# Performance work log

Measured on AMD Instinct MI355X. Metric: run time of the kernel, lower is better.

The kernel has to match this reference:

```python
import jax, jax.numpy as jnp
import numpy as np

B, C, H, W = 16, 256, 64, 64
NUM_HEADS = 4
GROUPS = 8
EPS = 1e-5


def setup_inputs() -> dict:
    key = jax.random.key(0)
    ks = jax.random.split(key, 7)
    x = jax.random.normal(ks[0], (B, C, H, W), dtype=jnp.float32)
    # GroupNorm affine params (torch default: weight=1, bias=0; randomize slightly for a stronger test)
    norm_w = jnp.ones((C,), jnp.float32) + 0.1 * jax.random.normal(ks[1], (C,), jnp.float32)
    norm_b = 0.1 * jax.random.normal(ks[2], (C,), jnp.float32)
    # 1x1 convs == channel GEMMs; kaiming-uniform-ish init scale
    s = 1.0 / np.sqrt(C)
    qkv_w = jax.random.uniform(ks[3], (3 * C, C), jnp.float32, -s, s)
    qkv_b = jax.random.uniform(ks[4], (3 * C,), jnp.float32, -s, s)
    proj_w = jax.random.uniform(ks[5], (C, C), jnp.float32, -s, s)
    proj_b = jax.random.uniform(ks[6], (C,), jnp.float32, -s, s)
    return {"x": x, "norm_w": norm_w, "norm_b": norm_b,
            "qkv_w": qkv_w, "qkv_b": qkv_b, "proj_w": proj_w, "proj_b": proj_b}


def reference(x, norm_w, norm_b, qkv_w, qkv_b, proj_w, proj_b):
    b, c, h, w = x.shape
    nh = NUM_HEADS
    dh = c // nh
    n = h * w
    # GroupNorm(8, C)
    xg = x.reshape(b, GROUPS, c // GROUPS, h, w)
    mean = xg.mean(axis=(2, 3, 4), keepdims=True)
    var = xg.var(axis=(2, 3, 4), keepdims=True)
    xn = ((xg - mean) * jax.lax.rsqrt(var + EPS)).reshape(b, c, h, w)
    xn = xn * norm_w[None, :, None, None] + norm_b[None, :, None, None]
    # QKV 1x1 conv as channel GEMM
    qkv = jnp.einsum('bchw,oc->bohw', xn, qkv_w) + qkv_b[None, :, None, None]
    qkv = qkv.reshape(b, 3, nh, dh, n)
    q, k, v = qkv[:, 0], qkv[:, 1], qkv[:, 2]  # each (B, nh, dh, N)
    scale = dh ** (-0.5)
    # Faithful to original einsum labeling: contracts over spatial axis,
    # attention matrix is over the HEADS axis: attn (B, dh, nh, nh)
    attn = jnp.einsum('bnhd,bmhd->bhnm', q * scale, k)
    attn = jax.nn.softmax(attn, axis=-1)
    out = jnp.einsum('bhnm,bmhd->bnhd', attn, v).reshape(b, c, h, w)
    return jnp.einsum('bchw,oc->bohw', out, proj_w) + proj_b[None, :, None, None] + x
```

## Files before the change

kernel.cpp:

```cpp
#include <hip/hip_runtime.h>
#include <stdint.h>

#define BB 16
#define CC 256
#define PP 4096

typedef __attribute__((ext_vector_type(4))) float f32x4;
typedef __attribute__((ext_vector_type(8))) short bf16x8;

static __device__ __forceinline__ float bf2f(unsigned short u) {
    union { uint32_t i; float f; } w; w.i = ((uint32_t)u) << 16; return w.f;
}
static __device__ __forceinline__ unsigned short f2bf(float f) {
    union { float f; uint32_t i; } w; w.f = f;
    uint32_t u = w.i;
    uint32_t r = u + 0x7FFFu + ((u >> 16) & 1u);
    return (unsigned short)(r >> 16);
}
static __device__ __forceinline__ float dot4(f32x4 a, f32x4 b) {
    return a.x * b.x + a.y * b.y + a.z * b.z + a.w * b.w;
}

static __device__ __forceinline__ void gl2lds16(const void* g, void* l) {
    __builtin_amdgcn_global_load_lds(
        (const __attribute__((address_space(1))) void*)g,
        (__attribute__((address_space(3))) void*)l, 16, 0, 0);
}

__global__ void gn_partial_k(const float* __restrict__ x, float* __restrict__ Sx,
                             float* __restrict__ Sxx) {
    int ch0 = blockIdx.x * 8;
    int t = threadIdx.x;
    int lc = t >> 5, l32 = t & 31;
    int ch = ch0 + lc;
    const f32x4* v = (const f32x4*)(x + (size_t)ch * PP);
    float s = 0.f, ss = 0.f;
    for (int i = l32; i < PP / 4; i += 32) {
        f32x4 tv = v[i];
        s  += tv.x + tv.y + tv.z + tv.w;
        ss += tv.x * tv.x + tv.y * tv.y + tv.z * tv.z + tv.w * tv.w;
    }
    for (int off = 16; off > 0; off >>= 1) {
        s  += __shfl_down(s, off, 32);
        ss += __shfl_down(ss, off, 32);
    }
    if (l32 == 0) { Sx[ch] = s; Sxx[ch] = ss; }
}

__global__ void gn_final_k(const float* __restrict__ Sx, const float* __restrict__ Sxx,
                           const float* __restrict__ nw, const float* __restrict__ nb,
                           float* __restrict__ a_s, float* __restrict__ b_s,
                           float* __restrict__ s_vec) {
    int b = blockIdx.x, c = threadIdx.x;
    __shared__ float lsx[256], lsxx[256];
    float mySx = Sx[b * CC + c];
    lsx[c] = mySx; lsxx[c] = Sxx[b * CC + c];
    __syncthreads();
    int g0 = (c >> 5) << 5;
    float S = 0.f, SS = 0.f;
    for (int j = 0; j < 32; j++) { S += lsx[g0 + j]; SS += lsxx[g0 + j]; }
    const float inv = 1.0f / 131072.0f;
    float mean = S * inv;
    float var = SS * inv - mean * mean;
    float rstd = rsqrtf(var + 1e-5f);
    float w = nw[c];
    float a = rstd * w;
    float sh = nb[c] - mean * rstd * w;
    a_s[b * CC + c] = a;
    b_s[b * CC + c] = sh;
    s_vec[b * CC + c] = a * mySx + 4096.0f * sh;
}

__global__ void cvt_bf16_k(const float* __restrict__ in, unsigned short* __restrict__ out, int n) {
    int i = blockIdx.x * 256 + threadIdx.x;
    if (i < n) out[i] = f2bf(in[i]);
}

__global__ void xnt_k(const float* __restrict__ x, const float* __restrict__ a_s,
                      const float* __restrict__ b_s, unsigned short* __restrict__ xnT,
                      unsigned short* __restrict__ xnC) {
    int pt = blockIdx.x & 63, ct = (blockIdx.x >> 6) & 3, b = blockIdx.x >> 8;
    int c0 = ct * 64, p0 = pt * 64;
    __shared__ unsigned short T[64][66];
    int t = threadIdx.x;
    int cl = t >> 4, pl4 = (t & 15) * 4;
    for (int i = 0; i < 4; i++) {
        int c = c0 + i * 16 + cl;
        float a = a_s[b * CC + c], sh = b_s[b * CC + c];
        f32x4 v = *(const f32x4*)(x + ((size_t)b * CC + c) * PP + p0 + pl4);
        ushort4 u;
        u.x = f2bf(a * v.x + sh);
        u.y = f2bf(a * v.y + sh);
        u.z = f2bf(a * v.z + sh);
        u.w = f2bf(a * v.w + sh);
        T[i * 16 + cl][pl4 + 0] = u.x;
        T[i * 16 + cl][pl4 + 1] = u.y;
        T[i * 16 + cl][pl4 + 2] = u.z;
        T[i * 16 + cl][pl4 + 3] = u.w;
        *(ushort4*)(xnC + ((size_t)b * CC + c) * PP + p0 + pl4) = u;
    }
    __syncthreads();
    int pl = t >> 2, c16 = (t & 3) * 16;
    union { unsigned short h[16]; uint4 u[2]; } buf;
    for (int j = 0; j < 16; j++) buf.h[j] = T[c16 + j][pl];
    unsigned short* dst = xnT + ((size_t)b * PP + p0 + pl) * CC + c0 + c16;
    *(uint4*)dst       = buf.u[0];
    *(uint4*)(dst + 8) = buf.u[1];
}

static __device__ __forceinline__ void gemm_core(const unsigned short* __restrict__ Rg,
                                                 const unsigned short* __restrict__ Cg,
                                                 int kLen, int rstride,
                                                 f32x4 (&acc)[4][4]) {
    __shared__ unsigned short Rs[128][32];
    __shared__ unsigned short Cs[128][32];
    int t = threadIdx.x;
    int lane = t & 63, wave = t >> 6;
    int wm = wave >> 1, wn = wave & 1;
    int lr = lane & 15, lq = lane >> 4;
    int srow = t >> 2;
    int ssl = (((t & 3) ^ ((t >> 3) & 3))) * 8;
    int fsw = (lr >> 1) & 3;
    for (int mi = 0; mi < 4; mi++)
        for (int ni = 0; ni < 4; ni++) {
            acc[mi][ni][0] = 0.f; acc[mi][ni][1] = 0.f;
            acc[mi][ni][2] = 0.f; acc[mi][ni][3] = 0.f;
        }
    const unsigned short* gr0 = Rg + (size_t)srow * rstride + ssl;
    const unsigned short* gr1 = gr0 + (size_t)64 * rstride;
    const unsigned short* gc0 = Cg + (size_t)srow * rstride + ssl;
    const unsigned short* gc1 = gc0 + (size_t)64 * rstride;
    char* dr0 = (char*)&Rs[0][0] + t * 16;
    char* dr1 = dr0 + 4096;
    char* dc0 = (char*)&Cs[0][0] + t * 16;
    char* dc1 = dc0 + 4096;
    for (int k0 = 0; k0 < kLen; k0 += 32) {
        __syncthreads();
        gl2lds16(gr0 + k0, dr0);
        gl2lds16(gr1 + k0, dr1);
        gl2lds16(gc0 + k0, dc0);
        gl2lds16(gc1 + k0, dc1);
        __syncthreads();
        bf16x8 af[4], bfr[4];
        for (int mi = 0; mi < 4; mi++)
            af[mi]  = *(const bf16x8*)&Rs[wm * 64 + mi * 16 + lr][(lq ^ fsw) * 8];
        for (int ni = 0; ni < 4; ni++)
            bfr[ni] = *(const bf16x8*)&Cs[wn * 64 + ni * 16 + lr][(lq ^ fsw) * 8];
        for (int mi = 0; mi < 4; mi++)
            for (int ni = 0; ni < 4; ni++)
                acc[mi][ni] = __builtin_amdgcn_mfma_f32_16x16x32_bf16(af[mi], bfr[ni], acc[mi][ni], 0, 0, 0);
    }
}

__global__ __launch_bounds__(256) void v_gemm_k(const unsigned short* __restrict__ Wvb,
                                                const unsigned short* __restrict__ xnT,
                                                const float* __restrict__ qkv_b,
                                                unsigned short* __restrict__ vT) {
    int nt = blockIdx.x & 31;
    int rest = blockIdx.x >> 5;
    int mt = rest & 1;
    int b  = rest >> 1;
    int c0 = mt * 128, p0 = nt * 128;
    f32x4 acc[4][4];
    gemm_core(Wvb + (size_t)c0 * 256, xnT + ((size_t)b * PP + p0) * 256, 256, 256, acc);
    int t = threadIdx.x, lane = t & 63, wave = t >> 6;
    int wm = wave >> 1, wn = wave & 1, lr = lane & 15, lq = lane >> 4;
    for (int mi = 0; mi < 4; mi++) {
        int c4 = c0 + wm * 64 + mi * 16 + lq * 4;
        f32x4 bias = *(const f32x4*)(qkv_b + 512 + c4);
        for (int ni = 0; ni < 4; ni++) {
            int p = p0 + wn * 64 + ni * 16 + lr;
            ushort4 u;
            u.x = f2bf(acc[mi][ni][0] + bias.x);
            u.y = f2bf(acc[mi][ni][1] + bias.y);
            u.z = f2bf(acc[mi][ni][2] + bias.z);
            u.w = f2bf(acc[mi][ni][3] + bias.w);
            *(ushort4*)(vT + ((size_t)b * PP + p) * CC + c4) = u;
        }
    }
}

__global__ __launch_bounds__(256) void gram_k(const unsigned short* __restrict__ xnC,
                                              float* __restrict__ Gpart) {
    int pc  = blockIdx.x & 7;
    int t12 = (blockIdx.x >> 3) & 3;
    int b   = blockIdx.x >> 5;
    int t1 = (t12 >> 1) * 128;
    int t2 = (t12 & 1) * 128;
    f32x4 acc[4][4];
    gemm_core(xnC + ((size_t)b * CC + t2) * PP + pc * 512,
              xnC + ((size_t)b * CC + t1) * PP + pc * 512, 512, PP, acc);
    int t = threadIdx.x, lane = t & 63, wave = t >> 6;
    int wm = wave >> 1, wn = wave & 1, lr = lane & 15, lq = lane >> 4;
    float* dst = Gpart + ((size_t)(pc * 16 + b)) * 65536;
    for (int mi = 0; mi < 4; mi++) {
        int c2q = t2 + wm * 64 + mi * 16 + lq * 4;
        for (int ni = 0; ni < 4; ni++) {
            int c1 = t1 + wn * 64 + ni * 16 + lr;
            *(f32x4*)(dst + (size_t)c1 * 256 + c2q) = acc[mi][ni];
        }
    }
}

__global__ void greduce_k(const float* __restrict__ Gpart, unsigned short* __restrict__ Gb) {
    int i = blockIdx.x * 256 + threadIdx.x;
    float s = 0.f;
    for (int pc = 0; pc < 8; pc++) s += Gpart[(size_t)pc * 16 * 65536 + i];
    Gb[i] = f2bf(s);
}

__global__ __launch_bounds__(256) void u_gemm_k(const unsigned short* __restrict__ Gb,
                                                const unsigned short* __restrict__ Wqkvb,
                                                float* __restrict__ UT) {
    int t12 = blockIdx.x & 3, b = blockIdx.x >> 2;
    int t1 = (t12 >> 1) * 128;
    int t2 = (t12 & 1) * 128;
    f32x4 acc[4][4];
    gemm_core(Gb + ((size_t)b * 256 + t1) * 256,
              Wqkvb + (size_t)(256 + t2) * 256, 256, 256, acc);
    int t = threadIdx.x, lane = t & 63, wave = t >> 6;
    int wm = wave >> 1, wn = wave & 1, lr = lane & 15, lq = lane >> 4;
    for (int mi = 0; mi < 4; mi++) {
        int c1q = t1 + wm * 64 + mi * 16 + lq * 4;
        for (int ni = 0; ni < 4; ni++) {
            int kr = t2 + wn * 64 + ni * 16 + lr;
            *(f32x4*)(UT + ((size_t)b * 256 + kr) * 256 + c1q) = acc[mi][ni];
        }
    }
}

__global__ void scoresfin_k(const float* __restrict__ qkv_w, const float* __restrict__ qkv_b,
                            const float* __restrict__ UT, const float* __restrict__ s_vec,
                            float* __restrict__ attn) {
    int h = blockIdx.x & 63, b = blockIdx.x >> 6;
    int l = threadIdx.x;
    int c = l * 4;
    f32x4 sv = *(const f32x4*)(s_vec + b * CC + c);
    f32x4 wq[4], wk[4], ut[4];
    for (int n = 0; n < 4; n++) wq[n] = *(const f32x4*)(qkv_w + (size_t)(n * 64 + h) * 256 + c);
    for (int m = 0; m < 4; m++) wk[m] = *(const f32x4*)(qkv_w + (size_t)(256 + m * 64 + h) * 256 + c);
    for (int m = 0; m < 4; m++) ut[m] = *(const f32x4*)(UT + ((size_t)b * 256 + m * 64 + h) * 256 + c);
    float red[24];
    for (int n = 0; n < 4; n++)
        for (int m = 0; m < 4; m++) red[n * 4 + m] = dot4(wq[n], ut[m]);
    for (int n = 0; n < 4; n++) red[16 + n] = dot4(wq[n], sv);
    for (int m = 0; m < 4; m++) red[20 + m] = dot4(wk[m], sv);
    #pragma unroll
    for (int i = 0; i < 24; i++)
        for (int off = 32; off > 0; off >>= 1)
            red[i] += __shfl_xor(red[i], off);
    __shared__ float sred[24];
    if (l == 0)
        for (int i = 0; i < 24; i++) sred[i] = red[i];
    __syncthreads();
    if (l < 4) {
        int n = l;
        float bq = qkv_b[n * 64 + h];
        float dqn = sred[16 + n];
        float lg[4];
        for (int m = 0; m < 4; m++) {
            float bk = qkv_b[256 + m * 64 + h];
            lg[m] = 0.125f * (sred[n * 4 + m] + bq * sred[20 + m] + bk * dqn + 4096.0f * bq * bk);
        }
        float mx = fmaxf(fmaxf(lg[0], lg[1]), fmaxf(lg[2], lg[3]));
        float e0 = expf(lg[0] - mx), e1 = expf(lg[1] - mx);
        float e2 = expf(lg[2] - mx), e3 = expf(lg[3] - mx);
        float inv = 1.0f / (e0 + e1 + e2 + e3);
        float* dst = attn + ((size_t)(b * 64 + h) * 4 + n) * 4;
        dst[0] = e0 * inv; dst[1] = e1 * inv; dst[2] = e2 * inv; dst[3] = e3 * inv;
    }
}

__global__ void make_wp_k(const float* __restrict__ proj_w, const float* __restrict__ attn,
                          unsigned short* __restrict__ Wp) {
    int t = threadIdx.x;
    int o = blockIdx.x & 255, b = blockIdx.x >> 8;
    int m = t >> 6, hh = t & 63;
    float s = 0.f;
    for (int n = 0; n < 4; n++)
        s += proj_w[o * 256 + n * 64 + hh] * attn[((size_t)(b * 64 + hh) * 4 + n) * 4 + m];
    Wp[((size_t)b * 256 + o) * 256 + t] = f2bf(s);
}

__global__ __launch_bounds__(256) void final_gemm_k(const unsigned short* __restrict__ Wp,
                                                    const unsigned short* __restrict__ vT,
                                                    const float* __restrict__ proj_b,
                                                    const float* __restrict__ x,
                                                    float* __restrict__ out) {
    int nt = blockIdx.x & 31;
    int rest = blockIdx.x >> 5;
    int mt = rest & 1;
    int b  = rest >> 1;
    int o0 = mt * 128, p0 = nt * 128;
    f32x4 acc[4][4];
    gemm_core(vT + ((size_t)b * PP + p0) * 256, Wp + ((size_t)b * 256 + o0) * 256, 256, 256, acc);
    int t = threadIdx.x, lane = t & 63, wave = t >> 6;
    int wm = wave >> 1, wn = wave & 1, lr = lane & 15, lq = lane >> 4;
    for (int mi = 0; mi < 4; mi++) {
        int p4 = p0 + wm * 64 + mi * 16 + lq * 4;
        for (int ni = 0; ni < 4; ni++) {
            int o = o0 + wn * 64 + ni * 16 + lr;
            size_t idx = ((size_t)b * CC + o) * PP + p4;
            float bias = proj_b[o];
            f32x4 xv = *(const f32x4*)(x + idx);
            f32x4 r;
            r[0] = acc[mi][ni][0] + bias + xv[0];
            r[1] = acc[mi][ni][1] + bias + xv[1];
            r[2] = acc[mi][ni][2] + bias + xv[2];
            r[3] = acc[mi][ni][3] + bias + xv[3];
            *(f32x4*)(out + idx) = r;
        }
    }
}

extern "C" void kernel_launch(void* const* d_in, const int* in_sizes, int n_in,
                              void* d_out, int out_size, void* d_ws, size_t ws_size,
                              hipStream_t stream) {
    const float* x      = (const float*)d_in[0];
    const float* norm_w = (const float*)d_in[1];
    const float* norm_b = (const float*)d_in[2];
    const float* qkv_w  = (const float*)d_in[3];
    const float* qkv_b  = (const float*)d_in[4];
    const float* proj_w = (const float*)d_in[5];
    const float* proj_b = (const float*)d_in[6];
    float* out = (float*)d_out;

    char* ws = (char*)d_ws;
    size_t off = 0;
    auto alloc = [&](size_t bytes) {
        void* p = ws + off;
        off += (bytes + 255) & ~(size_t)255;
        return p;
    };
    float* Sx    = (float*)alloc(BB * CC * sizeof(float));
    float* Sxx   = (float*)alloc(BB * CC * sizeof(float));
    float* a_s   = (float*)alloc(BB * CC * sizeof(float));
    float* b_s   = (float*)alloc(BB * CC * sizeof(float));
    float* s_vec = (float*)alloc(BB * CC * sizeof(float));
    float* attn  = (float*)alloc((size_t)BB * 64 * 16 * sizeof(float));
    unsigned short* Wqkvb = (unsigned short*)alloc((size_t)768 * 256 * 2);
    unsigned short* Wp    = (unsigned short*)alloc((size_t)BB * 256 * 256 * 2);
    unsigned short* Gb    = (unsigned short*)alloc((size_t)BB * 65536 * 2);
    float*          UT    = (float*)alloc((size_t)BB * 65536 * 4);
    float*          Gpart = (float*)alloc((size_t)8 * BB * 65536 * 4);
    unsigned short* xnT   = (unsigned short*)alloc((size_t)BB * PP * CC * 2);
    unsigned short* xnC   = (unsigned short*)alloc((size_t)BB * PP * CC * 2);
    unsigned short* vT    = (unsigned short*)alloc((size_t)BB * PP * CC * 2);

    gn_partial_k<<<BB * CC / 8, 256, 0, stream>>>(x, Sx, Sxx);
    gn_final_k<<<BB, 256, 0, stream>>>(Sx, Sxx, norm_w, norm_b, a_s, b_s, s_vec);
    cvt_bf16_k<<<768, 256, 0, stream>>>(qkv_w, Wqkvb, 768 * 256);
    xnt_k<<<4096, 256, 0, stream>>>(x, a_s, b_s, xnT, xnC);
    v_gemm_k<<<BB * 2 * 32, 256, 0, stream>>>(Wqkvb + 512 * 256, xnT, qkv_b, vT);
    gram_k<<<BB * 4 * 8, 256, 0, stream>>>(xnC, Gpart);
    greduce_k<<<BB * 65536 / 256, 256, 0, stream>>>(Gpart, Gb);
    u_gemm_k<<<BB * 4, 256, 0, stream>>>(Gb, Wqkvb, UT);
    scoresfin_k<<<BB * 64, 64, 0, stream>>>(qkv_w, qkv_b, UT, s_vec, attn);
    make_wp_k<<<BB * 256, 256, 0, stream>>>(proj_w, attn, Wp);
    final_gemm_k<<<BB * 2 * 32, 256, 0, stream>>>(Wp, vT, proj_b, x, out);
}
```

Measured before the change: 270.2 us.

## Fold V projection into per-batch output weights and drop the V GEMM

Removes the separate V GEMM and its bf16 vT intermediate. The V weights, transposed, are pre-multiplied into the per-batch attention-projection matrix (Wc = Wp·Wv) with a small per-batch GEMM, and the V bias is folded into a per-batch output bias. The final GEMM then consumes the normalized input directly. The shared GEMM core also switches from direct global-to-LDS loads to register-staged prefetching of the next K tile, and several kernels get a min-blocks launch bound of 3. The folding adds extra bf16 rounding of the combined weights.

Result: faster. 242.2 us (-10.3%).

```diff
diff --git a/kernel.cpp b/kernel.cpp
--- a/kernel.cpp
+++ b/kernel.cpp
@@ -19,12 +19,6 @@
 }
 static __device__ __forceinline__ float dot4(f32x4 a, f32x4 b) {
     return a.x * b.x + a.y * b.y + a.z * b.z + a.w * b.w;
-}
-
-static __device__ __forceinline__ void gl2lds16(const void* g, void* l) {
-    __builtin_amdgcn_global_load_lds(
-        (const __attribute__((address_space(1))) void*)g,
-        (__attribute__((address_space(3))) void*)l, 16, 0, 0);
 }
 
 __global__ void gn_partial_k(const float* __restrict__ x, float* __restrict__ Sx,
@@ -74,6 +68,27 @@
 __global__ void cvt_bf16_k(const float* __restrict__ in, unsigned short* __restrict__ out, int n) {
     int i = blockIdx.x * 256 + threadIdx.x;
     if (i < n) out[i] = f2bf(in[i]);
+}
+
+__global__ void wvt_k(const float* __restrict__ Wv, unsigned short* __restrict__ WvT) {
+    int tc1 = blockIdx.x & 3, tc2 = blockIdx.x >> 2;
+    int c1_0 = tc1 * 64, c2_0 = tc2 * 64;
+    __shared__ unsigned short T[64][65];
+    int t = threadIdx.x;
+    int r = t >> 2, q = (t & 3) * 16;
+    for (int j = 0; j < 4; j++) {
+        f32x4 v = *(const f32x4*)(Wv + (size_t)(c1_0 + r) * 256 + c2_0 + q + j * 4);
+        T[r][q + j * 4 + 0] = f2bf(v.x);
+        T[r][q + j * 4 + 1] = f2bf(v.y);
+        T[r][q + j * 4 + 2] = f2bf(v.z);
+        T[r][q + j * 4 + 3] = f2bf(v.w);
+    }
+    __syncthreads();
+    union { unsigned short h[16]; uint4 u[2]; } buf;
+    for (int j = 0; j < 16; j++) buf.h[j] = T[q + j][r];
+    unsigned short* dst = WvT + (size_t)(c2_0 + r) * 256 + c1_0 + q;
+    *(uint4*)dst       = buf.u[0];
+    *(uint4*)(dst + 8) = buf.u[1];
 }
 
 __global__ void xnt_k(const float* __restrict__ x, const float* __restrict__ a_s,
@@ -119,7 +134,8 @@
     int wm = wave >> 1, wn = wave & 1;
     int lr = lane & 15, lq = lane >> 4;
     int srow = t >> 2;
-    int ssl = (((t & 3) ^ ((t >> 3) & 3))) * 8;
+    int ssl = ((t & 3) ^ ((t >> 3) & 3)) * 8;
+    int sd  = (t & 3) * 8;
     int fsw = (lr >> 1) & 3;
     for (int mi = 0; mi < 4; mi++)
         for (int ni = 0; ni < 4; ni++) {
@@ -130,17 +146,24 @@
     const unsigned short* gr1 = gr0 + (size_t)64 * rstride;
     const unsigned short* gc0 = Cg + (size_t)srow * rstride + ssl;
     const unsigned short* gc1 = gc0 + (size_t)64 * rstride;
-    char* dr0 = (char*)&Rs[0][0] + t * 16;
-    char* dr1 = dr0 + 4096;
-    char* dc0 = (char*)&Cs[0][0] + t * 16;
-    char* dc1 = dc0 + 4096;
+    uint4 ra0 = *(const uint4*)(gr0);
+    uint4 ra1 = *(const uint4*)(gr1);
+    uint4 rc0 = *(const uint4*)(gc0);
+    uint4 rc1 = *(const uint4*)(gc1);
     for (int k0 = 0; k0 < kLen; k0 += 32) {
         __syncthreads();
-        gl2lds16(gr0 + k0, dr0);
-        gl2lds16(gr1 + k0, dr1);
-        gl2lds16(gc0 + k0, dc0);
-        gl2lds16(gc1 + k0, dc1);
+        *(uint4*)&Rs[srow][sd]      = ra0;
+        *(uint4*)&Rs[srow + 64][sd] = ra1;
+        *(uint4*)&Cs[srow][sd]      = rc0;
+        *(uint4*)&Cs[srow + 64][sd] = rc1;
         __syncthreads();
+        int kn = k0 + 32;
+        if (kn < kLen) {
+            ra0 = *(const uint4*)(gr0 + kn);
+            ra1 = *(const uint4*)(gr1 + kn);
+            rc0 = *(const uint4*)(gc0 + kn);
+            rc1 = *(const uint4*)(gc1 + kn);
+        }
         bf16x8 af[4], bfr[4];
         for (int mi = 0; mi < 4; mi++)
             af[mi]  = *(const bf16x8*)&Rs[wm * 64 + mi * 16 + lr][(lq ^ fsw) * 8];
@@ -152,36 +175,8 @@
     }
 }
 
-__global__ __launch_bounds__(256) void v_gemm_k(const unsigned short* __restrict__ Wvb,
-                                                const unsigned short* __restrict__ xnT,
-                                                const float* __restrict__ qkv_b,
-                                                unsigned short* __restrict__ vT) {
-    int nt = blockIdx.x & 31;
-    int rest = blockIdx.x >> 5;
-    int mt = rest & 1;
-    int b  = rest >> 1;
-    int c0 = mt * 128, p0 = nt * 128;
-    f32x4 acc[4][4];
-    gemm_core(Wvb + (size_t)c0 * 256, xnT + ((size_t)b * PP + p0) * 256, 256, 256, acc);
-    int t = threadIdx.x, lane = t & 63, wave = t >> 6;
-    int wm = wave >> 1, wn = wave & 1, lr = lane & 15, lq = lane >> 4;
-    for (int mi = 0; mi < 4; mi++) {
-        int c4 = c0 + wm * 64 + mi * 16 + lq * 4;
-        f32x4 bias = *(const f32x4*)(qkv_b + 512 + c4);
-        for (int ni = 0; ni < 4; ni++) {
-            int p = p0 + wn * 64 + ni * 16 + lr;
-            ushort4 u;
-            u.x = f2bf(acc[mi][ni][0] + bias.x);
-            u.y = f2bf(acc[mi][ni][1] + bias.y);
-            u.z = f2bf(acc[mi][ni][2] + bias.z);
-            u.w = f2bf(acc[mi][ni][3] + bias.w);
-            *(ushort4*)(vT + ((size_t)b * PP + p) * CC + c4) = u;
-        }
-    }
-}
-
-__global__ __launch_bounds__(256) void gram_k(const unsigned short* __restrict__ xnC,
-                                              float* __restrict__ Gpart) {
+__global__ __launch_bounds__(256, 3) void gram_k(const unsigned short* __restrict__ xnC,
+                                                 float* __restrict__ Gpart) {
     int pc  = blockIdx.x & 7;
     int t12 = (blockIdx.x >> 3) & 3;
     int b   = blockIdx.x >> 5;
@@ -209,9 +204,9 @@
     Gb[i] = f2bf(s);
 }
 
-__global__ __launch_bounds__(256) void u_gemm_k(const unsigned short* __restrict__ Gb,
-                                                const unsigned short* __restrict__ Wqkvb,
-                                                float* __restrict__ UT) {
+__global__ __launch_bounds__(256, 3) void u_gemm_k(const unsigned short* __restrict__ Gb,
+                                                   const unsigned short* __restrict__ Wqkvb,
+                                                   float* __restrict__ UT) {
     int t12 = blockIdx.x & 3, b = blockIdx.x >> 2;
     int t1 = (t12 >> 1) * 128;
     int t2 = (t12 & 1) * 128;
@@ -272,7 +267,8 @@
 }
 
 __global__ void make_wp_k(const float* __restrict__ proj_w, const float* __restrict__ attn,
-                          unsigned short* __restrict__ Wp) {
+                          const float* __restrict__ qkv_b, const float* __restrict__ proj_b,
+                          unsigned short* __restrict__ Wp, float* __restrict__ bias2) {
     int t = threadIdx.x;
     int o = blockIdx.x & 255, b = blockIdx.x >> 8;
     int m = t >> 6, hh = t & 63;
@@ -280,20 +276,51 @@
     for (int n = 0; n < 4; n++)
         s += proj_w[o * 256 + n * 64 + hh] * attn[((size_t)(b * 64 + hh) * 4 + n) * 4 + m];
     Wp[((size_t)b * 256 + o) * 256 + t] = f2bf(s);
-}
-
-__global__ __launch_bounds__(256) void final_gemm_k(const unsigned short* __restrict__ Wp,
-                                                    const unsigned short* __restrict__ vT,
-                                                    const float* __restrict__ proj_b,
-                                                    const float* __restrict__ x,
-                                                    float* __restrict__ out) {
+    float contrib = s * qkv_b[512 + t];
+    int lane = t & 63, wave = t >> 6;
+    for (int off = 32; off > 0; off >>= 1) contrib += __shfl_down(contrib, off);
+    __shared__ float red[4];
+    if (lane == 0) red[wave] = contrib;
+    __syncthreads();
+    if (t == 0) bias2[b * 256 + o] = proj_b[o] + red[0] + red[1] + red[2] + red[3];
+}
+
+__global__ __launch_bounds__(256, 3) void make_wc_k(const unsigned short* __restrict__ WvT,
+                                                    const unsigned short* __restrict__ Wp,
+                                                    unsigned short* __restrict__ Wc) {
+    int t12 = blockIdx.x & 3, b = blockIdx.x >> 2;
+    int c20 = (t12 & 1) * 128;
+    int o0  = (t12 >> 1) * 128;
+    f32x4 acc[4][4];
+    gemm_core(WvT + (size_t)c20 * 256, Wp + ((size_t)b * 256 + o0) * 256, 256, 256, acc);
+    int t = threadIdx.x, lane = t & 63, wave = t >> 6;
+    int wm = wave >> 1, wn = wave & 1, lr = lane & 15, lq = lane >> 4;
+    for (int mi = 0; mi < 4; mi++) {
+        int c2q = c20 + wm * 64 + mi * 16 + lq * 4;
+        for (int ni = 0; ni < 4; ni++) {
+            int o = o0 + wn * 64 + ni * 16 + lr;
+            ushort4 u;
+            u.x = f2bf(acc[mi][ni][0]);
+            u.y = f2bf(acc[mi][ni][1]);
+            u.z = f2bf(acc[mi][ni][2]);
+            u.w = f2bf(acc[mi][ni][3]);
+            *(ushort4*)(Wc + ((size_t)b * 256 + o) * 256 + c2q) = u;
+        }
+    }
+}
+
+__global__ __launch_bounds__(256, 3) void final_gemm_k(const unsigned short* __restrict__ Wc,
+                                                       const unsigned short* __restrict__ xnT,
+                                                       const float* __restrict__ bias2,
+                                                       const float* __restrict__ x,
+                                                       float* __restrict__ out) {
     int nt = blockIdx.x & 31;
     int rest = blockIdx.x >> 5;
     int mt = rest & 1;
     int b  = rest >> 1;
     int o0 = mt * 128, p0 = nt * 128;
     f32x4 acc[4][4];
-    gemm_core(vT + ((size_t)b * PP + p0) * 256, Wp + ((size_t)b * 256 + o0) * 256, 256, 256, acc);
+    gemm_core(xnT + ((size_t)b * PP + p0) * 256, Wc + ((size_t)b * 256 + o0) * 256, 256, 256, acc);
     int t = threadIdx.x, lane = t & 63, wave = t >> 6;
     int wm = wave >> 1, wn = wave & 1, lr = lane & 15, lq = lane >> 4;
     for (int mi = 0; mi < 4; mi++) {
@@ -301,7 +328,7 @@
         for (int ni = 0; ni < 4; ni++) {
             int o = o0 + wn * 64 + ni * 16 + lr;
             size_t idx = ((size_t)b * CC + o) * PP + p4;
-            float bias = proj_b[o];
+            float bias = bias2[b * CC + o];
             f32x4 xv = *(const f32x4*)(x + idx);
             f32x4 r;
             r[0] = acc[mi][ni][0] + bias + xv[0];
@@ -338,24 +365,27 @@
     float* b_s   = (float*)alloc(BB * CC * sizeof(float));
     float* s_vec = (float*)alloc(BB * CC * sizeof(float));
     float* attn  = (float*)alloc((size_t)BB * 64 * 16 * sizeof(float));
+    float* bias2 = (float*)alloc(BB * CC * sizeof(float));
     unsigned short* Wqkvb = (unsigned short*)alloc((size_t)768 * 256 * 2);
-    unsigned short* Wp    = (unsigned short*)alloc((size_t)BB * 256 * 256 * 2);
+    unsigned short* WvT   = (unsigned short*)alloc((size_t)256 * 256 * 2);
+    unsigned short* Wp    = (unsigned short*)alloc((size_t)BB * 65536 * 2);
+    unsigned short* Wc    = (unsigned short*)alloc((size_t)BB * 65536 * 2);
     unsigned short* Gb    = (unsigned short*)alloc((size_t)BB * 65536 * 2);
     float*          UT    = (float*)alloc((size_t)BB * 65536 * 4);
     float*          Gpart = (float*)alloc((size_t)8 * BB * 65536 * 4);
     unsigned short* xnT   = (unsigned short*)alloc((size_t)BB * PP * CC * 2);
     unsigned short* xnC   = (unsigned short*)alloc((size_t)BB * PP * CC * 2);
-    unsigned short* vT    = (unsigned short*)alloc((size_t)BB * PP * CC * 2);
 
     gn_partial_k<<<BB * CC / 8, 256, 0, stream>>>(x, Sx, Sxx);
     gn_final_k<<<BB, 256, 0, stream>>>(Sx, Sxx, norm_w, norm_b, a_s, b_s, s_vec);
     cvt_bf16_k<<<768, 256, 0, stream>>>(qkv_w, Wqkvb, 768 * 256);
+    wvt_k<<<16, 256, 0, stream>>>(qkv_w + (size_t)512 * 256, WvT);
     xnt_k<<<4096, 256, 0, stream>>>(x, a_s, b_s, xnT, xnC);
-    v_gemm_k<<<BB * 2 * 32, 256, 0, stream>>>(Wqkvb + 512 * 256, xnT, qkv_b, vT);
     gram_k<<<BB * 4 * 8, 256, 0, stream>>>(xnC, Gpart);
     greduce_k<<<BB * 65536 / 256, 256, 0, stream>>>(Gpart, Gb);
     u_gemm_k<<<BB * 4, 256, 0, stream>>>(Gb, Wqkvb, UT);
     scoresfin_k<<<BB * 64, 64, 0, stream>>>(qkv_w, qkv_b, UT, s_vec, attn);
-    make_wp_k<<<BB * 256, 256, 0, stream>>>(proj_w, attn, Wp);
-    final_gemm_k<<<BB * 2 * 32, 256, 0, stream>>>(Wp, vT, proj_b, x, out);
-}
+    make_wp_k<<<BB * 256, 256, 0, stream>>>(proj_w, attn, qkv_b, proj_b, Wp, bias2);
+    make_wc_k<<<BB * 4, 256, 0, stream>>>(WvT, Wp, Wc);
+    final_gemm_k<<<BB * 2 * 32, 256, 0, stream>>>(Wc, xnT, bias2, x, out);
+}
```
